# Optimization experiments

Measured on AMD Instinct MI355X. Metric: run time of the kernel, lower is better.

## Reference

```python
import jax, jax.numpy as jnp
import numpy as np

B, D, E, T = 262144, 128, 8, 3   # batch, input_dim, num_experts, num_tasks
H1, H2, G = 64, 32, 64           # expert hidden dims, gate hidden dim


def setup_inputs() -> dict:
    key = jax.random.key(0)
    ks = jax.random.split(key, 9)
    s = 0.05
    return {
        "x":   jax.random.normal(ks[0], (B, D), dtype=jnp.float32),
        # stacked expert MLP params: D -> H1 (relu) -> H2 (relu)
        "We1": jax.random.normal(ks[1], (E, D, H1), dtype=jnp.float32) * s,
        "be1": jax.random.normal(ks[2], (E, H1), dtype=jnp.float32) * s,
        "We2": jax.random.normal(ks[3], (E, H1, H2), dtype=jnp.float32) * s,
        "be2": jax.random.normal(ks[4], (E, H2), dtype=jnp.float32) * s,
        # stacked gate MLP params: D -> G (relu) -> E (linear, then softmax)
        "Wg1": jax.random.normal(ks[5], (T, D, G), dtype=jnp.float32) * s,
        "bg1": jax.random.normal(ks[6], (T, G), dtype=jnp.float32) * s,
        "Wg2": jax.random.normal(ks[7], (T, G, E), dtype=jnp.float32) * s,
        "bg2": jax.random.normal(ks[8], (T, E), dtype=jnp.float32) * s,
    }


def reference(x, We1, be1, We2, be2, Wg1, bg1, Wg2, bg2):
    # All experts as one batched GEMM chain: [B,E,H1] -> [B,E,H2]
    h1 = jax.nn.relu(jnp.einsum('bd,edh->beh', x, We1) + be1)
    experts_out = jax.nn.relu(jnp.einsum('beh,eho->beo', h1, We2) + be2)  # [B,E,H2]
    # All task gates as one batched GEMM chain: [B,T,E]
    g = jax.nn.relu(jnp.einsum('bd,tdh->bth', x, Wg1) + bg1)
    gate = jax.nn.softmax(jnp.einsum('bth,the->bte', g, Wg2) + bg2, axis=-1)
    # softmax-weighted sum over experts, per task
    out = jnp.einsum('bte,beo->bto', gate, experts_out)  # [B,T,H2]
    return tuple(out[:, t] for t in range(T))
```

## Files before the change

kernel.cpp:

```cpp
#include <hip/hip_runtime.h>

#define BROWS 262144
#define OUT_TASK_F32 8388608

#define WS_L1F 0
#define WS_L2F 196608
#define WS_B1  235520
#define WS_B2  238592

#define H1B 0
#define EOB 24576
#define SGB 40960
#define XSB 42496
#define LDS_TOTAL 50688

typedef __attribute__((ext_vector_type(8))) short bf16x8;
typedef __attribute__((ext_vector_type(4))) float f32x4;
typedef __attribute__((ext_vector_type(2))) unsigned int u32x2;

#define MFMA16(a, b, c) __builtin_amdgcn_mfma_f32_16x16x32_bf16((a), (b), (c), 0, 0, 0)

__device__ __forceinline__ unsigned short f2bf(float f) {
  unsigned int u = __float_as_uint(f);
  return (unsigned short)((u + 0x7FFFu + ((u >> 16) & 1u)) >> 16);
}
__device__ __forceinline__ unsigned int cvtpk(float lo, float hi) {
  unsigned int r;
  asm("v_cvt_pk_bf16_f32 %0, %1, %2" : "=v"(r) : "v"(lo), "v"(hi));
  return r;
}

__global__ void pack_kernel(const float* __restrict__ We1, const float* __restrict__ be1,
                            const float* __restrict__ We2, const float* __restrict__ be2,
                            const float* __restrict__ Wg1, const float* __restrict__ bg1,
                            const float* __restrict__ Wg2, const float* __restrict__ bg2,
                            unsigned char* __restrict__ ws) {
  int idx = blockIdx.x * blockDim.x + threadIdx.x;
  unsigned short* L1F = (unsigned short*)(ws + WS_L1F);
  unsigned short* L2F = (unsigned short*)(ws + WS_L2F);
  float* B1 = (float*)(ws + WS_B1);
  float* B2 = (float*)(ws + WS_B2);
  if (idx < 98304) {
    int j = idx & 7, lane = (idx >> 3) & 63, ks = (idx >> 9) & 3, nt = idx >> 11;
    int k = ks * 32 + ((lane >> 4) << 3) + j;
    int n = nt * 16 + (lane & 15);
    float v = 0.f;
    if (n < 512)      v = We1[((n >> 6) * 128 + k) * 64 + (n & 63)];
    else if (n < 704) v = Wg1[(((n - 512) >> 6) * 128 + k) * 64 + ((n - 512) & 63)];
    L1F[idx] = f2bf(v);
  } else if (idx < 98304 + 19456) {
    int i2 = idx - 98304;
    int j = i2 & 7, lane = (i2 >> 3) & 63, ks = (i2 >> 9) & 1, nt = i2 >> 10;
    int k = ks * 32 + ((lane >> 4) << 3) + j;
    int n = nt * 16 + (lane & 15);
    float v = 0.f;
    if (n < 256) v = We2[((n >> 5) * 64 + k) * 32 + (n & 31)];
    else { int g = n - 256, t = g >> 4, eo = g & 15; if (eo < 8) v = Wg2[(t * 64 + k) * 8 + eo]; }
    L2F[i2] = f2bf(v);
  } else if (idx < 98304 + 19456 + 768) {
    int n = idx - (98304 + 19456);
    float v = 0.f;
    if (n < 512)      v = be1[n];
    else if (n < 704) v = bg1[n - 512];
    B1[n] = v;
  } else if (idx < 98304 + 19456 + 768 + 304) {
    int n = idx - (98304 + 19456 + 768);
    float v = 0.f;
    if (n < 256) v = be2[n];
    else { int g = n - 256, t = g >> 4, eo = g & 15; if (eo < 8) v = Wg2 ? (eo < 8 ? bg2[t * 8 + eo] : 0.f) : 0.f;
           if (eo >= 8) v = 0.f; else v = bg2[t * 8 + eo]; }
    B2[n] = v;
  }
}

__global__ __launch_bounds__(512, 2) void mmoe_kernel(const float* __restrict__ x,
                                                      const unsigned char* __restrict__ ws,
                                                      float* __restrict__ out) {
  __shared__ unsigned char lds[LDS_TOTAL];

  const int tid = threadIdx.x;
  const int l   = tid & 63;
  const int wid = tid >> 6;
  const int l15 = l & 15;
  const int lhi = l >> 4;
  const int swz = (l15 & 7) << 4;

  const bf16x8* L1F = (const bf16x8*)(ws + WS_L1F);
  const bf16x8* L2F = (const bf16x8*)(ws + WS_L2F);
  const float*  B1  = (const float*)(ws + WS_B1);
  const float*  B2  = (const float*)(ws + WS_B2);

  int ntb[6];
#pragma unroll
  for (int i = 0; i < 6; ++i) ntb[i] = wid * 6 + i;
  if (wid >= 6) {
    int b = wid - 6;
#pragma unroll
    for (int i = 0; i < 4; ++i) ntb[i] = 36 + b * 4 + i;
    ntb[4] = 44 + b * 2; ntb[5] = 45 + b * 2;
  }

  bf16x8 w1f[6][4];
  f32x4 b1v[6];
#pragma unroll
  for (int i = 0; i < 6; ++i) {
#pragma unroll
    for (int ks = 0; ks < 4; ++ks) w1f[i][ks] = L1F[(ntb[i] * 4 + ks) * 64 + l];
    b1v[i] = *(const f32x4*)(B1 + ntb[i] * 16 + lhi * 4);
  }
  bf16x8 w2f[2][2];
  f32x4 b2v[2];
#pragma unroll
  for (int i = 0; i < 2; ++i) {
#pragma unroll
    for (int ks = 0; ks < 2; ++ks) w2f[i][ks] = L2F[((wid * 2 + i) * 2 + ks) * 64 + l];
    b2v[i] = *(const f32x4*)(B2 + wid * 32 + i * 16 + lhi * 4);
  }
  bf16x8 wgf[2];
  f32x4 bgv = (f32x4){0.f, 0.f, 0.f, 0.f};
  if (wid >= 5) {
    int t = wid - 5;
#pragma unroll
    for (int ks = 0; ks < 2; ++ks) wgf[ks] = L2F[((16 + t) * 2 + ks) * 64 + l];
    bgv = *(const f32x4*)(B2 + 256 + t * 16 + lhi * 4);
  }

  const int srow = tid >> 5, sk4 = tid & 31;
  const int rowbase = blockIdx.x * 1024;
  const int sswz = (srow & 7) << 4;

  {
    float4 sv = *(const float4*)(x + (size_t)(rowbase + srow) * 128 + sk4 * 4);
    u32x2 p; p[0] = cvtpk(sv.x, sv.y); p[1] = cvtpk(sv.z, sv.w);
    *(u32x2*)(lds + XSB + ((srow * 256 + sk4 * 8) ^ sswz)) = p;
  }
  __syncthreads();

  int cur = 0;
#pragma unroll 1
  for (int it = 0; it < 64; ++it) {
    float4 sv;
    const bool stage = (it + 1 < 64);
    if (stage)
      sv = *(const float4*)(x + (size_t)(rowbase + (it + 1) * 16 + srow) * 128 + sk4 * 4);

    if (it > 0 && wid < 6) {
      int t = wid >> 1, hf = wid & 1;
      f32x4 pA = *(const f32x4*)(lds + SGB + l15 * 96 + t * 32);
      f32x4 pB = *(const f32x4*)(lds + SGB + l15 * 96 + t * 32 + 16);
      f32x4 vac = (f32x4){0.f, 0.f, 0.f, 0.f};
#pragma unroll
      for (int e = 0; e < 4; ++e)
        vac += pA[e] * (*(const f32x4*)(lds + EOB + l15 * 1024 + ((e * 128 + hf * 64 + lhi * 16) ^ swz)));
#pragma unroll
      for (int e = 0; e < 4; ++e)
        vac += pB[e] * (*(const f32x4*)(lds + EOB + l15 * 1024 + (((e + 4) * 128 + hf * 64 + lhi * 16) ^ swz)));
      float* op = out + (size_t)t * OUT_TASK_F32 +
                  (size_t)(rowbase + (it - 1) * 16 + l15) * 32 + hf * 16 + lhi * 4;
      *(float4*)op = (float4){vac[0], vac[1], vac[2], vac[3]};
    }

    bf16x8 xa[4];
#pragma unroll
    for (int ks = 0; ks < 4; ++ks)
      xa[ks] = *(const bf16x8*)(lds + XSB + cur * 4096 + l15 * 256 + ((ks * 64 + lhi * 16) ^ swz));

    f32x4 acc[6];
#pragma unroll
    for (int i = 0; i < 6; ++i) acc[i] = b1v[i];
#pragma unroll
    for (int ks = 0; ks < 4; ++ks)
#pragma unroll
      for (int i = 0; i < 6; ++i)
        acc[i] = MFMA16(w1f[i][ks], xa[ks], acc[i]);

#pragma unroll
    for (int i = 0; i < 6; ++i) {
      float h0 = fmaxf(acc[i][0], 0.f), h1 = fmaxf(acc[i][1], 0.f);
      float h2 = fmaxf(acc[i][2], 0.f), h3 = fmaxf(acc[i][3], 0.f);
      u32x2 p; p[0] = cvtpk(h0, h1); p[1] = cvtpk(h2, h3);
      *(u32x2*)(lds + H1B + l15 * 1536 + ((ntb[i] * 32 + lhi * 8) ^ swz)) = p;
    }
    __syncthreads();

    bf16x8 hb0 = *(const bf16x8*)(lds + H1B + l15 * 1536 + ((wid * 128 + lhi * 16) ^ swz));
    bf16x8 hb1 = *(const bf16x8*)(lds + H1B + l15 * 1536 + ((wid * 128 + 64 + lhi * 16) ^ swz));
    f32x4 a2[2] = {b2v[0], b2v[1]};
#pragma unroll
    for (int i = 0; i < 2; ++i) {
      a2[i] = MFMA16(w2f[i][0], hb0, a2[i]);
      a2[i] = MFMA16(w2f[i][1], hb1, a2[i]);
      f32x4 r;
      r[0] = fmaxf(a2[i][0], 0.f); r[1] = fmaxf(a2[i][1], 0.f);
      r[2] = fmaxf(a2[i][2], 0.f); r[3] = fmaxf(a2[i][3], 0.f);
      *(f32x4*)(lds + EOB + l15 * 1024 + ((wid * 128 + i * 64 + lhi * 16) ^ swz)) = r;
    }

    if (wid >= 5) {
      int t = wid - 5;
      bf16x8 gb0 = *(const bf16x8*)(lds + H1B + l15 * 1536 + ((1024 + t * 128 + lhi * 16) ^ swz));
      bf16x8 gb1 = *(const bf16x8*)(lds + H1B + l15 * 1536 + ((1024 + t * 128 + 64 + lhi * 16) ^ swz));
      f32x4 ag = bgv;
      ag = MFMA16(wgf[0], gb0, ag);
      ag = MFMA16(wgf[1], gb1, ag);
      float s0 = ag[0], s1 = ag[1], s2 = ag[2], s3 = ag[3];
      float o0 = __shfl_xor(s0, 16), o1 = __shfl_xor(s1, 16);
      float o2 = __shfl_xor(s2, 16), o3 = __shfl_xor(s3, 16);
      float m = fmaxf(fmaxf(fmaxf(s0, s1), fmaxf(s2, s3)),
                      fmaxf(fmaxf(o0, o1), fmaxf(o2, o3)));
      float q0 = __expf(s0 - m), q1 = __expf(s1 - m), q2 = __expf(s2 - m), q3 = __expf(s3 - m);
      float ps = q0 + q1 + q2 + q3;
      float inv = 1.f / (ps + __shfl_xor(ps, 16));
      if (lhi < 2)
        *(f32x4*)(lds + SGB + l15 * 96 + t * 32 + lhi * 16) =
            (f32x4){q0 * inv, q1 * inv, q2 * inv, q3 * inv};
    }

    if (stage) {
      u32x2 p; p[0] = cvtpk(sv.x, sv.y); p[1] = cvtpk(sv.z, sv.w);
      *(u32x2*)(lds + XSB + (cur ^ 1) * 4096 + ((srow * 256 + sk4 * 8) ^ sswz)) = p;
    }
    __syncthreads();
    cur ^= 1;
  }

  if (wid < 6) {
    int t = wid >> 1, hf = wid & 1;
    f32x4 pA = *(const f32x4*)(lds + SGB + l15 * 96 + t * 32);
    f32x4 pB = *(const f32x4*)(lds + SGB + l15 * 96 + t * 32 + 16);
    f32x4 vac = (f32x4){0.f, 0.f, 0.f, 0.f};
#pragma unroll
    for (int e = 0; e < 4; ++e)
      vac += pA[e] * (*(const f32x4*)(lds + EOB + l15 * 1024 + ((e * 128 + hf * 64 + lhi * 16) ^ swz)));
#pragma unroll
    for (int e = 0; e < 4; ++e)
      vac += pB[e] * (*(const f32x4*)(lds + EOB + l15 * 1024 + (((e + 4) * 128 + hf * 64 + lhi * 16) ^ swz)));
    float* op = out + (size_t)t * OUT_TASK_F32 +
                (size_t)(rowbase + 63 * 16 + l15) * 32 + hf * 16 + lhi * 4;
    *(float4*)op = (float4){vac[0], vac[1], vac[2], vac[3]};
  }
}

extern "C" void kernel_launch(void* const* d_in, const int* in_sizes, int n_in,
                              void* d_out, int out_size, void* d_ws, size_t ws_size,
                              hipStream_t stream) {
  const float* x   = (const float*)d_in[0];
  const float* We1 = (const float*)d_in[1];
  const float* be1 = (const float*)d_in[2];
  const float* We2 = (const float*)d_in[3];
  const float* be2 = (const float*)d_in[4];
  const float* Wg1 = (const float*)d_in[5];
  const float* bg1 = (const float*)d_in[6];
  const float* Wg2 = (const float*)d_in[7];
  const float* bg2 = (const float*)d_in[8];
  unsigned char* ws = (unsigned char*)d_ws;
  float* out = (float*)d_out;

  pack_kernel<<<465, 256, 0, stream>>>(We1, be1, We2, be2, Wg1, bg1, Wg2, bg2, ws);
  mmoe_kernel<<<256, 512, 0, stream>>>(x, ws, out);
}
```

Baseline: 104.9 us.

## Software-pipeline layer1, layer2/gate, and mixing stages across iterations with double-buffered LDS

Restructures the per-tile loop into a three-stage software pipeline. Layer-1 MFMA for tile s, layer-2 plus gate softmax for tile s-1, and the softmax-weighted expert mix for tile s-2 all run in the same iteration, separated by a single barrier instead of two. H1, expert-output and gate buffers are double-buffered in LDS to make this possible, which raises LDS use from about 50KB to about 93KB per block. The aim is to halve barriers and let different waves overlap stages. The cost is that the larger LDS footprint may stop two 512-thread blocks from being resident per CU.

Result: no change. 103.2 us (-1.5%).

```diff
diff --git a/kernel.cpp b/kernel.cpp
--- a/kernel.cpp
+++ b/kernel.cpp
@@ -9,10 +9,10 @@
 #define WS_B2  238592
 
 #define H1B 0
-#define EOB 24576
-#define SGB 40960
-#define XSB 42496
-#define LDS_TOTAL 50688
+#define EOB 49152
+#define SGB 81920
+#define XSB 84992
+#define LDS_TOTAL 93184
 
 typedef __attribute__((ext_vector_type(8))) short bf16x8;
 typedef __attribute__((ext_vector_type(4))) float f32x4;
@@ -67,8 +67,7 @@
     int n = idx - (98304 + 19456 + 768);
     float v = 0.f;
     if (n < 256) v = be2[n];
-    else { int g = n - 256, t = g >> 4, eo = g & 15; if (eo < 8) v = Wg2 ? (eo < 8 ? bg2[t * 8 + eo] : 0.f) : 0.f;
-           if (eo >= 8) v = 0.f; else v = bg2[t * 8 + eo]; }
+    else { int g = n - 256, t = g >> 4, eo = g & 15; if (eo < 8) v = bg2[t * 8 + eo]; }
     B2[n] = v;
   }
 }
@@ -136,108 +135,97 @@
   }
   __syncthreads();
 
-  int cur = 0;
 #pragma unroll 1
-  for (int it = 0; it < 64; ++it) {
+  for (int s = 0; s < 66; ++s) {
+    const int pL1 = s & 1;
+    const int pL2 = (s - 1) & 1;
+
     float4 sv;
-    const bool stage = (it + 1 < 64);
+    const bool stage = (s + 1 < 64);
     if (stage)
-      sv = *(const float4*)(x + (size_t)(rowbase + (it + 1) * 16 + srow) * 128 + sk4 * 4);
-
-    if (it > 0 && wid < 6) {
+      sv = *(const float4*)(x + (size_t)(rowbase + (s + 1) * 16 + srow) * 128 + sk4 * 4);
+
+    if (s >= 2 && wid < 6) {
       int t = wid >> 1, hf = wid & 1;
-      f32x4 pA = *(const f32x4*)(lds + SGB + l15 * 96 + t * 32);
-      f32x4 pB = *(const f32x4*)(lds + SGB + l15 * 96 + t * 32 + 16);
+      f32x4 pA = *(const f32x4*)(lds + SGB + pL1 * 1536 + l15 * 96 + t * 32);
+      f32x4 pB = *(const f32x4*)(lds + SGB + pL1 * 1536 + l15 * 96 + t * 32 + 16);
       f32x4 vac = (f32x4){0.f, 0.f, 0.f, 0.f};
 #pragma unroll
       for (int e = 0; e < 4; ++e)
-        vac += pA[e] * (*(const f32x4*)(lds + EOB + l15 * 1024 + ((e * 128 + hf * 64 + lhi * 16) ^ swz)));
+        vac += pA[e] * (*(const f32x4*)(lds + EOB + pL1 * 16384 + l15 * 1024 +
+                                        ((e * 128 + hf * 64 + lhi * 16) ^ swz)));
 #pragma unroll
       for (int e = 0; e < 4; ++e)
-        vac += pB[e] * (*(const f32x4*)(lds + EOB + l15 * 1024 + (((e + 4) * 128 + hf * 64 + lhi * 16) ^ swz)));
+        vac += pB[e] * (*(const f32x4*)(lds + EOB + pL1 * 16384 + l15 * 1024 +
+                                        (((e + 4) * 128 + hf * 64 + lhi * 16) ^ swz)));
       float* op = out + (size_t)t * OUT_TASK_F32 +
-                  (size_t)(rowbase + (it - 1) * 16 + l15) * 32 + hf * 16 + lhi * 4;
+                  (size_t)(rowbase + (s - 2) * 16 + l15) * 32 + hf * 16 + lhi * 4;
       *(float4*)op = (float4){vac[0], vac[1], vac[2], vac[3]};
     }
 
-    bf16x8 xa[4];
-#pragma unroll
-    for (int ks = 0; ks < 4; ++ks)
-      xa[ks] = *(const bf16x8*)(lds + XSB + cur * 4096 + l15 * 256 + ((ks * 64 + lhi * 16) ^ swz));
-
-    f32x4 acc[6];
-#pragma unroll
-    for (int i = 0; i < 6; ++i) acc[i] = b1v[i];
-#pragma unroll
-    for (int ks = 0; ks < 4; ++ks)
-#pragma unroll
-      for (int i = 0; i < 6; ++i)
-        acc[i] = MFMA16(w1f[i][ks], xa[ks], acc[i]);
-
-#pragma unroll
-    for (int i = 0; i < 6; ++i) {
-      float h0 = fmaxf(acc[i][0], 0.f), h1 = fmaxf(acc[i][1], 0.f);
-      float h2 = fmaxf(acc[i][2], 0.f), h3 = fmaxf(acc[i][3], 0.f);
-      u32x2 p; p[0] = cvtpk(h0, h1); p[1] = cvtpk(h2, h3);
-      *(u32x2*)(lds + H1B + l15 * 1536 + ((ntb[i] * 32 + lhi * 8) ^ swz)) = p;
-    }
-    __syncthreads();
-
-    bf16x8 hb0 = *(const bf16x8*)(lds + H1B + l15 * 1536 + ((wid * 128 + lhi * 16) ^ swz));
-    bf16x8 hb1 = *(const bf16x8*)(lds + H1B + l15 * 1536 + ((wid * 128 + 64 + lhi * 16) ^ swz));
-    f32x4 a2[2] = {b2v[0], b2v[1]};
-#pragma unroll
-    for (int i = 0; i < 2; ++i) {
-      a2[i] = MFMA16(w2f[i][0], hb0, a2[i]);
-      a2[i] = MFMA16(w2f[i][1], hb1, a2[i]);
-      f32x4 r;
-      r[0] = fmaxf(a2[i][0], 0.f); r[1] = fmaxf(a2[i][1], 0.f);
-      r[2] = fmaxf(a2[i][2], 0.f); r[3] = fmaxf(a2[i][3], 0.f);
-      *(f32x4*)(lds + EOB + l15 * 1024 + ((wid * 128 + i * 64 + lhi * 16) ^ swz)) = r;
-    }
-
-    if (wid >= 5) {
-      int t = wid - 5;
-      bf16x8 gb0 = *(const bf16x8*)(lds + H1B + l15 * 1536 + ((1024 + t * 128 + lhi * 16) ^ swz));
-      bf16x8 gb1 = *(const bf16x8*)(lds + H1B + l15 * 1536 + ((1024 + t * 128 + 64 + lhi * 16) ^ swz));
-      f32x4 ag = bgv;
-      ag = MFMA16(wgf[0], gb0, ag);
-      ag = MFMA16(wgf[1], gb1, ag);
-      float s0 = ag[0], s1 = ag[1], s2 = ag[2], s3 = ag[3];
-      float o0 = __shfl_xor(s0, 16), o1 = __shfl_xor(s1, 16);
-      float o2 = __shfl_xor(s2, 16), o3 = __shfl_xor(s3, 16);
-      float m = fmaxf(fmaxf(fmaxf(s0, s1), fmaxf(s2, s3)),
-                      fmaxf(fmaxf(o0, o1), fmaxf(o2, o3)));
-      float q0 = __expf(s0 - m), q1 = __expf(s1 - m), q2 = __expf(s2 - m), q3 = __expf(s3 - m);
-      float ps = q0 + q1 + q2 + q3;
-      float inv = 1.f / (ps + __shfl_xor(ps, 16));
-      if (lhi < 2)
-        *(f32x4*)(lds + SGB + l15 * 96 + t * 32 + lhi * 16) =
-            (f32x4){q0 * inv, q1 * inv, q2 * inv, q3 * inv};
+    if (s < 64) {
+      bf16x8 xa[4];
+#pragma unroll
+      for (int ks = 0; ks < 4; ++ks)
+        xa[ks] = *(const bf16x8*)(lds + XSB + pL1 * 4096 + l15 * 256 +
+                                  ((ks * 64 + lhi * 16) ^ swz));
+      f32x4 acc[6];
+#pragma unroll
+      for (int i = 0; i < 6; ++i) acc[i] = b1v[i];
+#pragma unroll
+      for (int ks = 0; ks < 4; ++ks)
+#pragma unroll
+        for (int i = 0; i < 6; ++i)
+          acc[i] = MFMA16(w1f[i][ks], xa[ks], acc[i]);
+#pragma unroll
+      for (int i = 0; i < 6; ++i) {
+        u32x2 p;
+        p[0] = cvtpk(fmaxf(acc[i][0], 0.f), fmaxf(acc[i][1], 0.f));
+        p[1] = cvtpk(fmaxf(acc[i][2], 0.f), fmaxf(acc[i][3], 0.f));
+        *(u32x2*)(lds + H1B + pL1 * 24576 + l15 * 1536 + ((ntb[i] * 32 + lhi * 8) ^ swz)) = p;
+      }
+    }
+
+    if (s >= 1 && s < 65) {
+      bf16x8 hb0 = *(const bf16x8*)(lds + H1B + pL2 * 24576 + l15 * 1536 + ((wid * 128 + lhi * 16) ^ swz));
+      bf16x8 hb1 = *(const bf16x8*)(lds + H1B + pL2 * 24576 + l15 * 1536 + ((wid * 128 + 64 + lhi * 16) ^ swz));
+      f32x4 a2[2] = {b2v[0], b2v[1]};
+#pragma unroll
+      for (int i = 0; i < 2; ++i) {
+        a2[i] = MFMA16(w2f[i][0], hb0, a2[i]);
+        a2[i] = MFMA16(w2f[i][1], hb1, a2[i]);
+        f32x4 r;
+        r[0] = fmaxf(a2[i][0], 0.f); r[1] = fmaxf(a2[i][1], 0.f);
+        r[2] = fmaxf(a2[i][2], 0.f); r[3] = fmaxf(a2[i][3], 0.f);
+        *(f32x4*)(lds + EOB + pL2 * 16384 + l15 * 1024 + ((wid * 128 + i * 64 + lhi * 16) ^ swz)) = r;
+      }
+      if (wid >= 5) {
+        int t = wid - 5;
+        bf16x8 gb0 = *(const bf16x8*)(lds + H1B + pL2 * 24576 + l15 * 1536 + ((1024 + t * 128 + lhi * 16) ^ swz));
+        bf16x8 gb1 = *(const bf16x8*)(lds + H1B + pL2 * 24576 + l15 * 1536 + ((1024 + t * 128 + 64 + lhi * 16) ^ swz));
+        f32x4 ag = bgv;
+        ag = MFMA16(wgf[0], gb0, ag);
+        ag = MFMA16(wgf[1], gb1, ag);
+        float s0 = ag[0], s1 = ag[1], s2 = ag[2], s3 = ag[3];
+        float o0 = __shfl_xor(s0, 16), o1 = __shfl_xor(s1, 16);
+        float o2 = __shfl_xor(s2, 16), o3 = __shfl_xor(s3, 16);
+        float mx = fmaxf(fmaxf(fmaxf(s0, s1), fmaxf(s2, s3)),
+                         fmaxf(fmaxf(o0, o1), fmaxf(o2, o3)));
+        float q0 = __expf(s0 - mx), q1 = __expf(s1 - mx), q2 = __expf(s2 - mx), q3 = __expf(s3 - mx);
+        float ps = q0 + q1 + q2 + q3;
+        float inv = 1.f / (ps + __shfl_xor(ps, 16));
+        if (lhi < 2)
+          *(f32x4*)(lds + SGB + pL2 * 1536 + l15 * 96 + t * 32 + lhi * 16) =
+              (f32x4){q0 * inv, q1 * inv, q2 * inv, q3 * inv};
+      }
     }
 
     if (stage) {
       u32x2 p; p[0] = cvtpk(sv.x, sv.y); p[1] = cvtpk(sv.z, sv.w);
-      *(u32x2*)(lds + XSB + (cur ^ 1) * 4096 + ((srow * 256 + sk4 * 8) ^ sswz)) = p;
-    }
+      *(u32x2*)(lds + XSB + pL2 * 4096 + ((srow * 256 + sk4 * 8) ^ sswz)) = p;
+    }
+
     __syncthreads();
-    cur ^= 1;
-  }
-
-  if (wid < 6) {
-    int t = wid >> 1, hf = wid & 1;
-    f32x4 pA = *(const f32x4*)(lds + SGB + l15 * 96 + t * 32);
-    f32x4 pB = *(const f32x4*)(lds + SGB + l15 * 96 + t * 32 + 16);
-    f32x4 vac = (f32x4){0.f, 0.f, 0.f, 0.f};
-#pragma unroll
-    for (int e = 0; e < 4; ++e)
-      vac += pA[e] * (*(const f32x4*)(lds + EOB + l15 * 1024 + ((e * 128 + hf * 64 + lhi * 16) ^ swz)));
-#pragma unroll
-    for (int e = 0; e < 4; ++e)
-      vac += pB[e] * (*(const f32x4*)(lds + EOB + l15 * 1024 + (((e + 4) * 128 + hf * 64 + lhi * 16) ^ swz)));
-    float* op = out + (size_t)t * OUT_TASK_F32 +
-                (size_t)(rowbase + 63 * 16 + l15) * 32 + hf * 16 + lhi * 4;
-    *(float4*)op = (float4){vac[0], vac[1], vac[2], vac[3]};
   }
 }
 
```
